# Kernel optimization log

Hardware: AMD Instinct MI355X
Metric: run time of the kernel (lower is better)

The kernel has to match this reference:

```python
import jax, jax.numpy as jnp
import numpy as np

N = 100000      # nodes
E = 1600000     # edges
NFEAT = 200
NHID = 128
NOUT = 64
EPS = 1e-5      # BatchNorm eps


def setup_inputs() -> dict:
    key = jax.random.key(0)
    ks = jax.random.split(key, 12)

    def glorot(k, shape):
        fan_in, fan_out = shape
        lim = (6.0 / (fan_in + fan_out)) ** 0.5
        return jax.random.uniform(k, shape, jnp.float32, -lim, lim)

    return {
        "x": jax.random.normal(ks[0], (N, NFEAT), jnp.float32),
        "adj": jax.random.randint(ks[1], (2, E), 0, N, jnp.int64),
        "weight": jax.random.uniform(ks[2], (E,), jnp.float32),
        "W1": glorot(ks[3], (NFEAT, NHID)), "b1": jnp.zeros((NHID,), jnp.float32),
        "W2": glorot(ks[4], (NHID, NHID)), "b2": jnp.zeros((NHID,), jnp.float32),
        "g1": jnp.ones((NHID,), jnp.float32), "beta1": jnp.zeros((NHID,), jnp.float32),
        "g2": jnp.ones((NHID,), jnp.float32), "beta2": jnp.zeros((NHID,), jnp.float32),
        "fc1_W": glorot(ks[5], (NFEAT + 2 * NHID, NHID)), "fc1_b": jnp.zeros((NHID,), jnp.float32),
        "fc2_W": glorot(ks[6], (NHID, NOUT)), "fc2_b": jnp.zeros((NOUT,), jnp.float32),
    }


def gcn_conv(x, src, dst, ew, W, b):
    # PyG GCNConv: add self-loops (weight 1), symmetric normalization,
    # h = D^{-1/2} (A+I) D^{-1/2} (x W) + b. Aggregation at dst from src.
    h = x @ W                                   # [N, F_out]
    deg = jax.ops.segment_sum(ew, dst, num_segments=N)  # weighted in-degree (+1 self)
    dinv = jnp.where(deg > 0, jax.lax.rsqrt(deg), 0.0)
    norm = dinv[src] * ew * dinv[dst]           # [E+N]
    msg = h[src] * norm[:, None]                # [E+N, F_out] gather
    out = jax.ops.segment_sum(msg, dst, num_segments=N)  # scatter-add
    return out + b


def batch_norm(h, g, beta):
    m = h.mean(axis=0)
    v = jnp.mean(jnp.square(h - m), axis=0)
    return g * (h - m) * jax.lax.rsqrt(v + EPS) + beta


def reference(x, adj, weight, W1, b1, W2, b2, g1, beta1, g2, beta2,
              fc1_W, fc1_b, fc2_W, fc2_b):
    # add self-loops once (shared by both conv layers)
    loop = jnp.arange(N, dtype=adj.dtype)
    src = jnp.concatenate([adj[0], loop])
    dst = jnp.concatenate([adj[1], loop])
    ew = jnp.concatenate([weight, jnp.ones((N,), weight.dtype)])

    h1 = jax.nn.relu(gcn_conv(x, src, dst, ew, W1, b1))
    h1 = batch_norm(h1, g1, beta1)              # dropout = identity (eval)
    h2 = jax.nn.relu(gcn_conv(h1, src, dst, ew, W2, b2))
    h2 = batch_norm(h2, g2, beta2)

    cat = jnp.concatenate([x, h1, h2], axis=1)  # [N, nfeat + 2*nhid]
    out = jax.nn.relu(cat @ fc1_W + fc1_b)
    out = jax.nn.relu(out @ fc2_W + fc2_b)
    return out
```

## Files before the change

kernel.cpp:

```cpp
#include <hip/hip_runtime.h>
#include <hip/hip_bf16.h>

#define N_NODES 100000
#define N_EDGES 1600000
#define NFEAT   200
#define NHID    128
#define NOUT    64
#define BN_EPS  1e-5f

static constexpr int SCAN_NB = (N_NODES + 255) / 256;

__global__ __launch_bounds__(256) void init_kernel(int* counts, float* deg, float* stats)
{
    int i = blockIdx.x * 256 + threadIdx.x;
    if (i <= N_NODES) counts[i] = 0;
    if (i <  N_NODES) deg[i]    = 1.0f;
    if (i <  512)     stats[i]  = 0.0f;
}

__global__ __launch_bounds__(256) void hist_kernel(const int* __restrict__ adj,
                                                   const float* __restrict__ wt,
                                                   int* __restrict__ counts,
                                                   float* __restrict__ deg)
{
    int e = blockIdx.x * 256 + threadIdx.x;
    if (e >= N_EDGES) return;
    int d = adj[N_EDGES + e];
    atomicAdd(&counts[d], 1);
    atomicAdd(&deg[d], wt[e]);
}

__global__ __launch_bounds__(256) void scan_block(const int* __restrict__ counts,
                                                  int* __restrict__ rowptr,
                                                  int* __restrict__ bsums)
{
    __shared__ int s[256];
    int t = threadIdx.x;
    int i = blockIdx.x * 256 + t;
    int v = (i < N_NODES) ? counts[i] : 0;
    s[t] = v; __syncthreads();
    #pragma unroll
    for (int off = 1; off < 256; off <<= 1) {
        int x = (t >= off) ? s[t - off] : 0;
        __syncthreads();
        s[t] += x;
        __syncthreads();
    }
    if (i < N_NODES) rowptr[i] = s[t] - v;
    if (t == 255) bsums[blockIdx.x] = s[255];
}

__global__ __launch_bounds__(512) void scan_top(int* bsums)
{
    __shared__ int s[512];
    int t = threadIdx.x;
    int v = (t < SCAN_NB) ? bsums[t] : 0;
    s[t] = v; __syncthreads();
    #pragma unroll
    for (int off = 1; off < 512; off <<= 1) {
        int x = (t >= off) ? s[t - off] : 0;
        __syncthreads();
        s[t] += x;
        __syncthreads();
    }
    if (t < SCAN_NB) bsums[t] = s[t] - v;
}

__global__ __launch_bounds__(256) void scan_add(int* __restrict__ rowptr,
                                                const int* __restrict__ bsums,
                                                int* __restrict__ cursor,
                                                float* __restrict__ deg)
{
    int i = blockIdx.x * 256 + threadIdx.x;
    if (i < N_NODES) {
        int r = rowptr[i] + bsums[i >> 8];
        rowptr[i] = r;
        cursor[i] = r;
        float d = deg[i];
        deg[i] = (d > 0.f) ? rsqrtf(d) : 0.f;
    }
    if (i == 0) rowptr[N_NODES] = N_EDGES;
}

__global__ __launch_bounds__(256) void fill_kernel(const int* __restrict__ adj,
                                                   const float* __restrict__ wt,
                                                   const float* __restrict__ dinv,
                                                   int* __restrict__ cursor,
                                                   int2* __restrict__ col)
{
    int e = blockIdx.x * 256 + threadIdx.x;
    if (e >= N_EDGES) return;
    int s = adj[e];
    int d = adj[N_EDGES + e];
    int pos = atomicAdd(&cursor[d], 1);
    int2 c;
    c.x = s;
    c.y = __float_as_int(dinv[s] * wt[e] * dinv[d]);
    col[pos] = c;
}

template<int NC, bool BIASRELU, bool HASBN>
__global__ __launch_bounds__(256) void gemm_kernel(const float* __restrict__ A,
                                                   const float* __restrict__ W,
                                                   const float* __restrict__ bias,
                                                   const float* __restrict__ scsh,
                                                   float* __restrict__ C,
                                                   int M, int K)
{
    constexpr int BM = 128, BK = 64;
    constexpr int COLG = NC / 8;
    constexpr int RPT  = (BM * COLG) / 256;
    __shared__ float a_t[BM][BK + 2];
    __shared__ float w_t[BK][NC];

    int t    = threadIdx.x;
    int m0   = blockIdx.x * BM;
    int g    = t % COLG;
    int c_lo = g * 4;
    int c_hi = NC / 2 + c_lo;
    int r0   = (t / COLG) * RPT;

    float acc[RPT][8];
    #pragma unroll
    for (int j = 0; j < RPT; ++j)
        #pragma unroll
        for (int i = 0; i < 8; ++i) acc[j][i] = 0.f;

    for (int k0 = 0; k0 < K; k0 += BK) {
        constexpr int WF4 = BK * NC / 4 / 256;
        #pragma unroll
        for (int i = 0; i < WF4; ++i) {
            int idx = t + i * 256;
            int kr  = idx / (NC / 4);
            int c4  = (idx % (NC / 4)) * 4;
            float4 v = make_float4(0.f, 0.f, 0.f, 0.f);
            if (k0 + kr < K) v = *(const float4*)&W[(size_t)(k0 + kr) * NC + c4];
            *(float4*)&w_t[kr][c4] = v;
        }
        #pragma unroll
        for (int i = 0; i < BM * BK / 4 / 256; ++i) {
            int idx = t + i * 256;
            int ar  = idx / (BK / 4);
            int ac  = (idx % (BK / 4)) * 4;
            float4 v = make_float4(0.f, 0.f, 0.f, 0.f);
            int m = m0 + ar, k = k0 + ac;
            if (m < M && k < K) {
                v = *(const float4*)&A[(size_t)m * K + k];
                if (HASBN) {
                    float4 sc = *(const float4*)&scsh[k];
                    float4 sh = *(const float4*)&scsh[NHID + k];
                    v.x = v.x * sc.x + sh.x;
                    v.y = v.y * sc.y + sh.y;
                    v.z = v.z * sc.z + sh.z;
                    v.w = v.w * sc.w + sh.w;
                }
            }
            a_t[ar][ac]     = v.x;
            a_t[ar][ac + 1] = v.y;
            a_t[ar][ac + 2] = v.z;
            a_t[ar][ac + 3] = v.w;
        }
        __syncthreads();

        #pragma unroll 8
        for (int kk = 0; kk < BK; ++kk) {
            float4 w0 = *(float4*)&w_t[kk][c_lo];
            float4 w1 = *(float4*)&w_t[kk][c_hi];
            #pragma unroll
            for (int j = 0; j < RPT; ++j) {
                float a = a_t[r0 + j][kk];
                acc[j][0] += a * w0.x; acc[j][1] += a * w0.y;
                acc[j][2] += a * w0.z; acc[j][3] += a * w0.w;
                acc[j][4] += a * w1.x; acc[j][5] += a * w1.y;
                acc[j][6] += a * w1.z; acc[j][7] += a * w1.w;
            }
        }
        __syncthreads();
    }

    float4 b0, b1;
    if (BIASRELU) {
        b0 = *(const float4*)&bias[c_lo];
        b1 = *(const float4*)&bias[c_hi];
    }
    #pragma unroll
    for (int j = 0; j < RPT; ++j) {
        int m = m0 + r0 + j;
        if (m >= M) continue;
        float4 o0 = make_float4(acc[j][0], acc[j][1], acc[j][2], acc[j][3]);
        float4 o1 = make_float4(acc[j][4], acc[j][5], acc[j][6], acc[j][7]);
        if (BIASRELU) {
            o0.x = fmaxf(o0.x + b0.x, 0.f); o0.y = fmaxf(o0.y + b0.y, 0.f);
            o0.z = fmaxf(o0.z + b0.z, 0.f); o0.w = fmaxf(o0.w + b0.w, 0.f);
            o1.x = fmaxf(o1.x + b1.x, 0.f); o1.y = fmaxf(o1.y + b1.y, 0.f);
            o1.z = fmaxf(o1.z + b1.z, 0.f); o1.w = fmaxf(o1.w + b1.w, 0.f);
        }
        *(float4*)&C[(size_t)m * NC + c_lo] = o0;
        *(float4*)&C[(size_t)m * NC + c_hi] = o1;
    }
}

__global__ __launch_bounds__(256) void fc1_kernel(const float* __restrict__ x,
                                                  const float* __restrict__ h1,
                                                  const float* __restrict__ s1,
                                                  const float* __restrict__ h2,
                                                  const float* __restrict__ s2,
                                                  const float* __restrict__ W,
                                                  const float* __restrict__ bias,
                                                  float* __restrict__ C, int M)
{
    constexpr int NC = NHID, BM = 128, BK = 64, KTOT = NFEAT + 2 * NHID;
    constexpr int COLG = NC / 8, RPT = (BM * COLG) / 256;
    __shared__ float a_t[BM][BK + 2];
    __shared__ float w_t[BK][NC];

    int t    = threadIdx.x;
    int m0   = blockIdx.x * BM;
    int g    = t % COLG;
    int c_lo = g * 4;
    int c_hi = NC / 2 + c_lo;
    int r0   = (t / COLG) * RPT;

    float acc[RPT][8];
    #pragma unroll
    for (int j = 0; j < RPT; ++j)
        #pragma unroll
        for (int i = 0; i < 8; ++i) acc[j][i] = 0.f;

    for (int k0 = 0; k0 < 512; k0 += BK) {
        #pragma unroll
        for (int i = 0; i < 8; ++i) {
            int idx = t + i * 256;
            int kr  = idx / (NC / 4);
            int c4  = (idx % (NC / 4)) * 4;
            float4 v = make_float4(0.f, 0.f, 0.f, 0.f);
            if (k0 + kr < KTOT) v = *(const float4*)&W[(size_t)(k0 + kr) * NC + c4];
            *(float4*)&w_t[kr][c4] = v;
        }
        #pragma unroll
        for (int i = 0; i < BM * BK / 4 / 256; ++i) {
            int idx = t + i * 256;
            int ar  = idx / (BK / 4);
            int ac  = (idx % (BK / 4)) * 4;
            int m   = m0 + ar, kc = k0 + ac;
            float4 v = make_float4(0.f, 0.f, 0.f, 0.f);
            if (m < M) {
                if (kc < NFEAT) {
                    v = *(const float4*)&x[(size_t)m * NFEAT + kc];
                } else if (kc < NFEAT + NHID) {
                    int k = kc - NFEAT;
                    v = *(const float4*)&h1[(size_t)m * NHID + k];
                    float4 sc = *(const float4*)&s1[k];
                    float4 sh = *(const float4*)&s1[NHID + k];
                    v.x = v.x * sc.x + sh.x; v.y = v.y * sc.y + sh.y;
                    v.z = v.z * sc.z + sh.z; v.w = v.w * sc.w + sh.w;
                } else if (kc < KTOT) {
                    int k = kc - NFEAT - NHID;
                    v = *(const float4*)&h2[(size_t)m * NHID + k];
                    float4 sc = *(const float4*)&s2[k];
                    float4 sh = *(const float4*)&s2[NHID + k];
                    v.x = v.x * sc.x + sh.x; v.y = v.y * sc.y + sh.y;
                    v.z = v.z * sc.z + sh.z; v.w = v.w * sc.w + sh.w;
                }
            }
            a_t[ar][ac]     = v.x;
            a_t[ar][ac + 1] = v.y;
            a_t[ar][ac + 2] = v.z;
            a_t[ar][ac + 3] = v.w;
        }
        __syncthreads();

        #pragma unroll 8
        for (int kk = 0; kk < BK; ++kk) {
            float4 w0 = *(float4*)&w_t[kk][c_lo];
            float4 w1 = *(float4*)&w_t[kk][c_hi];
            #pragma unroll
            for (int j = 0; j < RPT; ++j) {
                float a = a_t[r0 + j][kk];
                acc[j][0] += a * w0.x; acc[j][1] += a * w0.y;
                acc[j][2] += a * w0.z; acc[j][3] += a * w0.w;
                acc[j][4] += a * w1.x; acc[j][5] += a * w1.y;
                acc[j][6] += a * w1.z; acc[j][7] += a * w1.w;
            }
        }
        __syncthreads();
    }

    float4 b0 = *(const float4*)&bias[c_lo];
    float4 b1 = *(const float4*)&bias[c_hi];
    #pragma unroll
    for (int j = 0; j < RPT; ++j) {
        int m = m0 + r0 + j;
        if (m >= M) continue;
        float4 o0 = make_float4(fmaxf(acc[j][0] + b0.x, 0.f), fmaxf(acc[j][1] + b0.y, 0.f),
                                fmaxf(acc[j][2] + b0.z, 0.f), fmaxf(acc[j][3] + b0.w, 0.f));
        float4 o1 = make_float4(fmaxf(acc[j][4] + b1.x, 0.f), fmaxf(acc[j][5] + b1.y, 0.f),
                                fmaxf(acc[j][6] + b1.z, 0.f), fmaxf(acc[j][7] + b1.w, 0.f));
        *(float4*)&C[(size_t)m * NC + c_lo] = o0;
        *(float4*)&C[(size_t)m * NC + c_hi] = o1;
    }
}

__global__ __launch_bounds__(256) void agg_kernel(const float* __restrict__ h,
                                                  const float* __restrict__ bias,
                                                  const float* __restrict__ dinv,
                                                  const int* __restrict__ rowptr,
                                                  const int2* __restrict__ col,
                                                  float* __restrict__ out)
{
    int node = blockIdx.x * 4 + (threadIdx.x >> 6);
    if (node >= N_NODES) return;
    int lane = threadIdx.x & 63;
    int f0 = lane * 2;

    float di = dinv[node];
    float2 hv = *(const float2*)&h[(size_t)node * NHID + f0];
    float ax = di * di * hv.x;
    float ay = di * di * hv.y;

    int e = rowptr[node], end = rowptr[node + 1];
    for (; e + 4 <= end; e += 4) {
        int2 c0 = col[e],     c1 = col[e + 1];
        int2 c2 = col[e + 2], c3 = col[e + 3];
        float2 v0 = *(const float2*)&h[(size_t)c0.x * NHID + f0];
        float2 v1 = *(const float2*)&h[(size_t)c1.x * NHID + f0];
        float2 v2 = *(const float2*)&h[(size_t)c2.x * NHID + f0];
        float2 v3 = *(const float2*)&h[(size_t)c3.x * NHID + f0];
        float n0 = __int_as_float(c0.y), n1 = __int_as_float(c1.y);
        float n2 = __int_as_float(c2.y), n3 = __int_as_float(c3.y);
        ax += n0 * v0.x + n1 * v1.x + n2 * v2.x + n3 * v3.x;
        ay += n0 * v0.y + n1 * v1.y + n2 * v2.y + n3 * v3.y;
    }
    for (; e < end; ++e) {
        int2 c = col[e];
        float2 v = *(const float2*)&h[(size_t)c.x * NHID + f0];
        float n = __int_as_float(c.y);
        ax += n * v.x;
        ay += n * v.y;
    }
    float2 b = *(const float2*)&bias[f0];
    float2 o;
    o.x = fmaxf(ax + b.x, 0.f);
    o.y = fmaxf(ay + b.y, 0.f);
    *(float2*)&out[(size_t)node * NHID + f0] = o;
}

__global__ __launch_bounds__(256) void stats_kernel(const float* __restrict__ h,
                                                    float* __restrict__ st)
{
    __shared__ float ls[256], ls2[256];
    int t = threadIdx.x;
    int c = t & 127, half = t >> 7;
    float s = 0.f, s2 = 0.f;
    for (int r = blockIdx.x * 2 + half; r < N_NODES; r += gridDim.x * 2) {
        float v = h[(size_t)r * NHID + c];
        s += v; s2 += v * v;
    }
    ls[t] = s; ls2[t] = s2; __syncthreads();
    if (half == 0) {
        s  += ls[t + 128];
        s2 += ls2[t + 128];
        atomicAdd(&st[c], s);
        atomicAdd(&st[128 + c], s2);
    }
}

__global__ __launch_bounds__(128) void bn_finalize(const float* __restrict__ st,
                                                   const float* __restrict__ g,
                                                   const float* __restrict__ beta,
                                                   float* __restrict__ scsh)
{
    int c = threadIdx.x;
    float mean = st[c] / (float)N_NODES;
    float var  = st[128 + c] / (float)N_NODES - mean * mean;
    float inv  = rsqrtf(var + BN_EPS);
    float sc   = g[c] * inv;
    scsh[c]        = sc;
    scsh[NHID + c] = beta[c] - mean * sc;
}

extern "C" void kernel_launch(void* const* d_in, const int* in_sizes, int n_in,
                              void* d_out, int out_size, void* d_ws, size_t ws_size,
                              hipStream_t stream)
{
    const float* x     = (const float*)d_in[0];
    const int*   adj   = (const int*)d_in[1];
    const float* wt    = (const float*)d_in[2];
    const float* W1    = (const float*)d_in[3];
    const float* b1    = (const float*)d_in[4];
    const float* W2    = (const float*)d_in[5];
    const float* b2    = (const float*)d_in[6];
    const float* g1    = (const float*)d_in[7];
    const float* beta1 = (const float*)d_in[8];
    const float* g2    = (const float*)d_in[9];
    const float* beta2 = (const float*)d_in[10];
    const float* fc1W  = (const float*)d_in[11];
    const float* fc1b  = (const float*)d_in[12];
    const float* fc2W  = (const float*)d_in[13];
    const float* fc2b  = (const float*)d_in[14];
    float* out = (float*)d_out;

    char* p = (char*)d_ws;
    auto alloc = [&](size_t bytes) -> void* {
        void* r = (void*)p;
        p += (bytes + 255) & ~(size_t)255;
        return r;
    };
    float* dinv   = (float*)alloc((size_t)N_NODES * 4);
    int*   counts = (int*)  alloc((size_t)(N_NODES + 1) * 4);
    int*   rowptr = (int*)  alloc((size_t)(N_NODES + 1) * 4);
    int*   cursor = (int*)  alloc((size_t)N_NODES * 4);
    int2*  col    = (int2*) alloc((size_t)N_EDGES * 8);
    int*   bsums  = (int*)  alloc(1024 * 4);
    float* stats  = (float*)alloc(512 * 4);
    float* scsh1  = (float*)alloc(256 * 4);
    float* scsh2  = (float*)alloc(256 * 4);
    float* t_buf  = (float*)alloc((size_t)N_NODES * NHID * 4);
    float* h1     = (float*)alloc((size_t)N_NODES * NHID * 4);
    float* h2     = (float*)alloc((size_t)N_NODES * NHID * 4);

    const int gN1 = (N_NODES + 256) / 256;
    const int gE  = (N_EDGES + 255) / 256;
    const int gM  = (N_NODES + 127) / 128;

    init_kernel<<<gN1, 256, 0, stream>>>(counts, dinv, stats);
    hist_kernel<<<gE, 256, 0, stream>>>(adj, wt, counts, dinv);
    scan_block<<<SCAN_NB, 256, 0, stream>>>(counts, rowptr, bsums);
    scan_top<<<1, 512, 0, stream>>>(bsums);
    scan_add<<<SCAN_NB, 256, 0, stream>>>(rowptr, bsums, cursor, dinv);
    fill_kernel<<<gE, 256, 0, stream>>>(adj, wt, dinv, cursor, col);

    gemm_kernel<NHID, false, false><<<gM, 256, 0, stream>>>(x, W1, nullptr, nullptr, t_buf, N_NODES, NFEAT);
    agg_kernel<<<(N_NODES + 3) / 4, 256, 0, stream>>>(t_buf, b1, dinv, rowptr, col, h1);
    stats_kernel<<<1024, 256, 0, stream>>>(h1, stats);
    bn_finalize<<<1, 128, 0, stream>>>(stats, g1, beta1, scsh1);

    gemm_kernel<NHID, false, true><<<gM, 256, 0, stream>>>(h1, W2, nullptr, scsh1, t_buf, N_NODES, NHID);
    agg_kernel<<<(N_NODES + 3) / 4, 256, 0, stream>>>(t_buf, b2, dinv, rowptr, col, h2);
    stats_kernel<<<1024, 256, 0, stream>>>(h2, stats + 256);
    bn_finalize<<<1, 128, 0, stream>>>(stats + 256, g2, beta2, scsh2);

    fc1_kernel<<<gM, 256, 0, stream>>>(x, h1, scsh1, h2, scsh2, fc1W, fc1b, t_buf, N_NODES);

    gemm_kernel<NOUT, true, false><<<gM, 256, 0, stream>>>(t_buf, fc2W, fc2b, nullptr, out, N_NODES, NHID);
}
```

Measured before the change: 1.259 ms.

## Fold BatchNorm into GEMM weights and stream A operands directly from global

```diff
diff --git a/kernel.cpp b/kernel.cpp
--- a/kernel.cpp
+++ b/kernel.cpp
@@ -99,26 +99,35 @@
     col[pos] = c;
 }
 
-template<int NC, bool BIASRELU, bool HASBN>
-__global__ __launch_bounds__(256) void gemm_kernel(const float* __restrict__ A,
-                                                   const float* __restrict__ W,
-                                                   const float* __restrict__ bias,
-                                                   const float* __restrict__ scsh,
-                                                   float* __restrict__ C,
-                                                   int M, int K)
-{
-    constexpr int BM = 128, BK = 64;
+template<int NC, bool RELU>
+__global__ __launch_bounds__(256) void gemm2(const float* __restrict__ A,
+                                             const float* __restrict__ W,
+                                             const float* __restrict__ bias,
+                                             float* __restrict__ C,
+                                             int M, int K)
+{
+    constexpr int BK   = 64;
     constexpr int COLG = NC / 8;
-    constexpr int RPT  = (BM * COLG) / 256;
-    __shared__ float a_t[BM][BK + 2];
+    constexpr int RG   = 256 / COLG;
+    constexpr int BM   = 128;
+    constexpr int RPT  = BM / RG;
     __shared__ float w_t[BK][NC];
 
-    int t    = threadIdx.x;
-    int m0   = blockIdx.x * BM;
-    int g    = t % COLG;
-    int c_lo = g * 4;
-    int c_hi = NC / 2 + c_lo;
-    int r0   = (t / COLG) * RPT;
+    const int t    = threadIdx.x;
+    const int m0   = blockIdx.x * BM;
+    const int g    = t % COLG;
+    const int c_lo = g * 4;
+    const int c_hi = NC / 2 + c_lo;
+    const int r0   = (t / COLG) * RPT;
+
+    bool rowok[RPT];
+    const float* arow[RPT];
+    #pragma unroll
+    for (int j = 0; j < RPT; ++j) {
+        int m = m0 + r0 + j;
+        rowok[j] = (m < M);
+        arow[j]  = A + (size_t)(rowok[j] ? m : 0) * K;
+    }
 
     float acc[RPT][8];
     #pragma unroll
@@ -127,7 +136,8 @@
         for (int i = 0; i < 8; ++i) acc[j][i] = 0.f;
 
     for (int k0 = 0; k0 < K; k0 += BK) {
-        constexpr int WF4 = BK * NC / 4 / 256;
+        __syncthreads();
+        constexpr int WF4 = BK * NC / 1024;
         #pragma unroll
         for (int i = 0; i < WF4; ++i) {
             int idx = t + i * 256;
@@ -137,49 +147,40 @@
             if (k0 + kr < K) v = *(const float4*)&W[(size_t)(k0 + kr) * NC + c4];
             *(float4*)&w_t[kr][c4] = v;
         }
-        #pragma unroll
-        for (int i = 0; i < BM * BK / 4 / 256; ++i) {
-            int idx = t + i * 256;
-            int ar  = idx / (BK / 4);
-            int ac  = (idx % (BK / 4)) * 4;
-            float4 v = make_float4(0.f, 0.f, 0.f, 0.f);
-            int m = m0 + ar, k = k0 + ac;
-            if (m < M && k < K) {
-                v = *(const float4*)&A[(size_t)m * K + k];
-                if (HASBN) {
-                    float4 sc = *(const float4*)&scsh[k];
-                    float4 sh = *(const float4*)&scsh[NHID + k];
-                    v.x = v.x * sc.x + sh.x;
-                    v.y = v.y * sc.y + sh.y;
-                    v.z = v.z * sc.z + sh.z;
-                    v.w = v.w * sc.w + sh.w;
+        __syncthreads();
+
+        #pragma unroll 4
+        for (int q = 0; q < BK / 4; ++q) {
+            int k = k0 + q * 4;
+            float4 a[RPT];
+            if (k < K) {
+                #pragma unroll
+                for (int j = 0; j < RPT; ++j)
+                    a[j] = rowok[j] ? *(const float4*)&arow[j][k]
+                                    : make_float4(0.f, 0.f, 0.f, 0.f);
+            } else {
+                #pragma unroll
+                for (int j = 0; j < RPT; ++j) a[j] = make_float4(0.f, 0.f, 0.f, 0.f);
+            }
+            #pragma unroll
+            for (int u = 0; u < 4; ++u) {
+                float4 w0 = *(const float4*)&w_t[q * 4 + u][c_lo];
+                float4 w1 = *(const float4*)&w_t[q * 4 + u][c_hi];
+                #pragma unroll
+                for (int j = 0; j < RPT; ++j) {
+                    float av = ((const float*)&a[j])[u];
+                    acc[j][0] += av * w0.x; acc[j][1] += av * w0.y;
+                    acc[j][2] += av * w0.z; acc[j][3] += av * w0.w;
+                    acc[j][4] += av * w1.x; acc[j][5] += av * w1.y;
+                    acc[j][6] += av * w1.z; acc[j][7] += av * w1.w;
                 }
             }
-            a_t[ar][ac]     = v.x;
-            a_t[ar][ac + 1] = v.y;
-            a_t[ar][ac + 2] = v.z;
-            a_t[ar][ac + 3] = v.w;
-        }
-        __syncthreads();
-
-        #pragma unroll 8
-        for (int kk = 0; kk < BK; ++kk) {
-            float4 w0 = *(float4*)&w_t[kk][c_lo];
-            float4 w1 = *(float4*)&w_t[kk][c_hi];
-            #pragma unroll
-            for (int j = 0; j < RPT; ++j) {
-                float a = a_t[r0 + j][kk];
-                acc[j][0] += a * w0.x; acc[j][1] += a * w0.y;
-                acc[j][2] += a * w0.z; acc[j][3] += a * w0.w;
-                acc[j][4] += a * w1.x; acc[j][5] += a * w1.y;
-                acc[j][6] += a * w1.z; acc[j][7] += a * w1.w;
-            }
-        }
-        __syncthreads();
-    }
-
-    float4 b0, b1;
-    if (BIASRELU) {
+        }
+    }
+
+    float4 b0 = make_float4(0.f, 0.f, 0.f, 0.f);
+    float4 b1 = make_float4(0.f, 0.f, 0.f, 0.f);
+    if (bias) {
         b0 = *(const float4*)&bias[c_lo];
         b1 = *(const float4*)&bias[c_hi];
     }
@@ -187,39 +188,47 @@
     for (int j = 0; j < RPT; ++j) {
         int m = m0 + r0 + j;
         if (m >= M) continue;
-        float4 o0 = make_float4(acc[j][0], acc[j][1], acc[j][2], acc[j][3]);
-        float4 o1 = make_float4(acc[j][4], acc[j][5], acc[j][6], acc[j][7]);
-        if (BIASRELU) {
-            o0.x = fmaxf(o0.x + b0.x, 0.f); o0.y = fmaxf(o0.y + b0.y, 0.f);
-            o0.z = fmaxf(o0.z + b0.z, 0.f); o0.w = fmaxf(o0.w + b0.w, 0.f);
-            o1.x = fmaxf(o1.x + b1.x, 0.f); o1.y = fmaxf(o1.y + b1.y, 0.f);
-            o1.z = fmaxf(o1.z + b1.z, 0.f); o1.w = fmaxf(o1.w + b1.w, 0.f);
+        float4 o0 = make_float4(acc[j][0] + b0.x, acc[j][1] + b0.y,
+                                acc[j][2] + b0.z, acc[j][3] + b0.w);
+        float4 o1 = make_float4(acc[j][4] + b1.x, acc[j][5] + b1.y,
+                                acc[j][6] + b1.z, acc[j][7] + b1.w);
+        if (RELU) {
+            o0.x = fmaxf(o0.x, 0.f); o0.y = fmaxf(o0.y, 0.f);
+            o0.z = fmaxf(o0.z, 0.f); o0.w = fmaxf(o0.w, 0.f);
+            o1.x = fmaxf(o1.x, 0.f); o1.y = fmaxf(o1.y, 0.f);
+            o1.z = fmaxf(o1.z, 0.f); o1.w = fmaxf(o1.w, 0.f);
         }
         *(float4*)&C[(size_t)m * NC + c_lo] = o0;
         *(float4*)&C[(size_t)m * NC + c_hi] = o1;
     }
 }
 
-__global__ __launch_bounds__(256) void fc1_kernel(const float* __restrict__ x,
-                                                  const float* __restrict__ h1,
-                                                  const float* __restrict__ s1,
-                                                  const float* __restrict__ h2,
-                                                  const float* __restrict__ s2,
-                                                  const float* __restrict__ W,
-                                                  const float* __restrict__ bias,
-                                                  float* __restrict__ C, int M)
-{
-    constexpr int NC = NHID, BM = 128, BK = 64, KTOT = NFEAT + 2 * NHID;
-    constexpr int COLG = NC / 8, RPT = (BM * COLG) / 256;
-    __shared__ float a_t[BM][BK + 2];
+__global__ __launch_bounds__(256) void gemm_cat(const float* __restrict__ x,
+                                                const float* __restrict__ h1,
+                                                const float* __restrict__ h2,
+                                                const float* __restrict__ Wf,
+                                                const float* __restrict__ bf,
+                                                float* __restrict__ C, int M)
+{
+    constexpr int NC = NHID, BK = 64, KTOT = NFEAT + 2 * NHID;
+    constexpr int COLG = 16, RPT = 8, BM = 128;
     __shared__ float w_t[BK][NC];
 
-    int t    = threadIdx.x;
-    int m0   = blockIdx.x * BM;
-    int g    = t % COLG;
-    int c_lo = g * 4;
-    int c_hi = NC / 2 + c_lo;
-    int r0   = (t / COLG) * RPT;
+    const int t    = threadIdx.x;
+    const int m0   = blockIdx.x * BM;
+    const int g    = t % COLG;
+    const int c_lo = g * 4;
+    const int c_hi = NC / 2 + c_lo;
+    const int r0   = (t / COLG) * RPT;
+
+    bool rowok[RPT];
+    int  mrow[RPT];
+    #pragma unroll
+    for (int j = 0; j < RPT; ++j) {
+        int m = m0 + r0 + j;
+        rowok[j] = (m < M);
+        mrow[j]  = rowok[j] ? m : 0;
+    }
 
     float acc[RPT][8];
     #pragma unroll
@@ -228,66 +237,53 @@
         for (int i = 0; i < 8; ++i) acc[j][i] = 0.f;
 
     for (int k0 = 0; k0 < 512; k0 += BK) {
+        __syncthreads();
         #pragma unroll
         for (int i = 0; i < 8; ++i) {
             int idx = t + i * 256;
             int kr  = idx / (NC / 4);
             int c4  = (idx % (NC / 4)) * 4;
             float4 v = make_float4(0.f, 0.f, 0.f, 0.f);
-            if (k0 + kr < KTOT) v = *(const float4*)&W[(size_t)(k0 + kr) * NC + c4];
+            if (k0 + kr < KTOT) v = *(const float4*)&Wf[(size_t)(k0 + kr) * NC + c4];
             *(float4*)&w_t[kr][c4] = v;
         }
-        #pragma unroll
-        for (int i = 0; i < BM * BK / 4 / 256; ++i) {
-            int idx = t + i * 256;
-            int ar  = idx / (BK / 4);
-            int ac  = (idx % (BK / 4)) * 4;
-            int m   = m0 + ar, kc = k0 + ac;
-            float4 v = make_float4(0.f, 0.f, 0.f, 0.f);
-            if (m < M) {
-                if (kc < NFEAT) {
-                    v = *(const float4*)&x[(size_t)m * NFEAT + kc];
-                } else if (kc < NFEAT + NHID) {
-                    int k = kc - NFEAT;
-                    v = *(const float4*)&h1[(size_t)m * NHID + k];
-                    float4 sc = *(const float4*)&s1[k];
-                    float4 sh = *(const float4*)&s1[NHID + k];
-                    v.x = v.x * sc.x + sh.x; v.y = v.y * sc.y + sh.y;
-                    v.z = v.z * sc.z + sh.z; v.w = v.w * sc.w + sh.w;
-                } else if (kc < KTOT) {
-                    int k = kc - NFEAT - NHID;
-                    v = *(const float4*)&h2[(size_t)m * NHID + k];
-                    float4 sc = *(const float4*)&s2[k];
-                    float4 sh = *(const float4*)&s2[NHID + k];
-                    v.x = v.x * sc.x + sh.x; v.y = v.y * sc.y + sh.y;
-                    v.z = v.z * sc.z + sh.z; v.w = v.w * sc.w + sh.w;
+        __syncthreads();
+
+        #pragma unroll 4
+        for (int q = 0; q < BK / 4; ++q) {
+            int kc = k0 + q * 4;
+            float4 a[RPT];
+            if (kc < KTOT) {
+                const float* src; int kk, ld;
+                if (kc < NFEAT)             { src = x;  kk = kc;               ld = NFEAT; }
+                else if (kc < NFEAT + NHID) { src = h1; kk = kc - NFEAT;       ld = NHID;  }
+                else                        { src = h2; kk = kc - NFEAT - NHID; ld = NHID; }
+                #pragma unroll
+                for (int j = 0; j < RPT; ++j)
+                    a[j] = rowok[j] ? *(const float4*)&src[(size_t)mrow[j] * ld + kk]
+                                    : make_float4(0.f, 0.f, 0.f, 0.f);
+            } else {
+                #pragma unroll
+                for (int j = 0; j < RPT; ++j) a[j] = make_float4(0.f, 0.f, 0.f, 0.f);
+            }
+            #pragma unroll
+            for (int u = 0; u < 4; ++u) {
+                float4 w0 = *(const float4*)&w_t[q * 4 + u][c_lo];
+                float4 w1 = *(const float4*)&w_t[q * 4 + u][c_hi];
+                #pragma unroll
+                for (int j = 0; j < RPT; ++j) {
+                    float av = ((const float*)&a[j])[u];
+                    acc[j][0] += av * w0.x; acc[j][1] += av * w0.y;
+                    acc[j][2] += av * w0.z; acc[j][3] += av * w0.w;
+                    acc[j][4] += av * w1.x; acc[j][5] += av * w1.y;
+                    acc[j][6] += av * w1.z; acc[j][7] += av * w1.w;
                 }
             }
-            a_t[ar][ac]     = v.x;
-            a_t[ar][ac + 1] = v.y;
-            a_t[ar][ac + 2] = v.z;
-            a_t[ar][ac + 3] = v.w;
-        }
-        __syncthreads();
-
-        #pragma unroll 8
-        for (int kk = 0; kk < BK; ++kk) {
-            float4 w0 = *(float4*)&w_t[kk][c_lo];
-            float4 w1 = *(float4*)&w_t[kk][c_hi];
-            #pragma unroll
-            for (int j = 0; j < RPT; ++j) {
-                float a = a_t[r0 + j][kk];
-                acc[j][0] += a * w0.x; acc[j][1] += a * w0.y;
-                acc[j][2] += a * w0.z; acc[j][3] += a * w0.w;
-                acc[j][4] += a * w1.x; acc[j][5] += a * w1.y;
-                acc[j][6] += a * w1.z; acc[j][7] += a * w1.w;
-            }
-        }
-        __syncthreads();
-    }
-
-    float4 b0 = *(const float4*)&bias[c_lo];
-    float4 b1 = *(const float4*)&bias[c_hi];
+        }
+    }
+
+    float4 b0 = *(const float4*)&bf[c_lo];
+    float4 b1 = *(const float4*)&bf[c_hi];
     #pragma unroll
     for (int j = 0; j < RPT; ++j) {
         int m = m0 + r0 + j;
@@ -298,6 +294,48 @@
                                 fmaxf(acc[j][6] + b1.z, 0.f), fmaxf(acc[j][7] + b1.w, 0.f));
         *(float4*)&C[(size_t)m * NC + c_lo] = o0;
         *(float4*)&C[(size_t)m * NC + c_hi] = o1;
+    }
+}
+
+__global__ __launch_bounds__(128) void wfold2(const float* __restrict__ W2,
+                                              const float* __restrict__ scsh1,
+                                              float* __restrict__ W2f,
+                                              float* __restrict__ c2)
+{
+    int c = threadIdx.x;
+    float acc = 0.f;
+    for (int k = 0; k < NHID; ++k) {
+        float w = W2[k * NHID + c];
+        W2f[k * NHID + c] = scsh1[k] * w;
+        acc += scsh1[NHID + k] * w;
+    }
+    c2[c] = acc;
+}
+
+__global__ __launch_bounds__(128) void fc1fold(const float* __restrict__ Wc,
+                                               const float* __restrict__ fc1b,
+                                               const float* __restrict__ scsh1,
+                                               const float* __restrict__ scsh2,
+                                               float* __restrict__ Wf,
+                                               float* __restrict__ bf)
+{
+    int c = threadIdx.x;
+    if (blockIdx.x == 0) {
+        for (int k = 0; k < NFEAT; ++k)
+            Wf[(size_t)k * NHID + c] = Wc[(size_t)k * NHID + c];
+    } else {
+        float acc = fc1b[c];
+        for (int k = 0; k < NHID; ++k) {
+            float w = Wc[(size_t)(NFEAT + k) * NHID + c];
+            Wf[(size_t)(NFEAT + k) * NHID + c] = scsh1[k] * w;
+            acc += scsh1[NHID + k] * w;
+        }
+        for (int k = 0; k < NHID; ++k) {
+            float w = Wc[(size_t)(NFEAT + NHID + k) * NHID + c];
+            Wf[(size_t)(NFEAT + NHID + k) * NHID + c] = scsh2[k] * w;
+            acc += scsh2[NHID + k] * w;
+        }
+        bf[c] = acc;
     }
 }
 
@@ -415,6 +453,10 @@
     float* stats  = (float*)alloc(512 * 4);
     float* scsh1  = (float*)alloc(256 * 4);
     float* scsh2  = (float*)alloc(256 * 4);
+    float* W2f    = (float*)alloc((size_t)NHID * NHID * 4);
+    float* c2b    = (float*)alloc(256 * 4);
+    float* Wf     = (float*)alloc((size_t)(NFEAT + 2 * NHID) * NHID * 4);
+    float* bf     = (float*)alloc(256 * 4);
     float* t_buf  = (float*)alloc((size_t)N_NODES * NHID * 4);
     float* h1     = (float*)alloc((size_t)N_NODES * NHID * 4);
     float* h2     = (float*)alloc((size_t)N_NODES * NHID * 4);
@@ -430,17 +472,19 @@
     scan_add<<<SCAN_NB, 256, 0, stream>>>(rowptr, bsums, cursor, dinv);
     fill_kernel<<<gE, 256, 0, stream>>>(adj, wt, dinv, cursor, col);
 
-    gemm_kernel<NHID, false, false><<<gM, 256, 0, stream>>>(x, W1, nullptr, nullptr, t_buf, N_NODES, NFEAT);
+    gemm2<NHID, false><<<gM, 256, 0, stream>>>(x, W1, nullptr, t_buf, N_NODES, NFEAT);
     agg_kernel<<<(N_NODES + 3) / 4, 256, 0, stream>>>(t_buf, b1, dinv, rowptr, col, h1);
     stats_kernel<<<1024, 256, 0, stream>>>(h1, stats);
     bn_finalize<<<1, 128, 0, stream>>>(stats, g1, beta1, scsh1);
 
-    gemm_kernel<NHID, false, true><<<gM, 256, 0, stream>>>(h1, W2, nullptr, scsh1, t_buf, N_NODES, NHID);
+    wfold2<<<1, 128, 0, stream>>>(W2, scsh1, W2f, c2b);
+    gemm2<NHID, false><<<gM, 256, 0, stream>>>(h1, W2f, c2b, t_buf, N_NODES, NHID);
     agg_kernel<<<(N_NODES + 3) / 4, 256, 0, stream>>>(t_buf, b2, dinv, rowptr, col, h2);
     stats_kernel<<<1024, 256, 0, stream>>>(h2, stats + 256);
     bn_finalize<<<1, 128, 0, stream>>>(stats + 256, g2, beta2, scsh2);
 
-    fc1_kernel<<<gM, 256, 0, stream>>>(x, h1, scsh1, h2, scsh2, fc1W, fc1b, t_buf, N_NODES);
-
-    gemm_kernel<NOUT, true, false><<<gM, 256, 0, stream>>>(t_buf, fc2W, fc2b, nullptr, out, N_NODES, NHID);
-}
+    fc1fold<<<2, 128, 0, stream>>>(fc1W, fc1b, scsh1, scsh2, Wf, bf);
+    gemm_cat<<<gM, 256, 0, stream>>>(x, h1, h2, Wf, bf, t_buf, N_NODES);
+
+    gemm2<NOUT, true><<<gM, 256, 0, stream>>>(t_buf, fc2W, fc2b, out, N_NODES, NHID);
+}
```

After: 2.101 ms. 66.9% more time.
